# Performance work log

Hardware: AMD Instinct MI355X
Metric: run time of the kernel (lower is better)

## Reference

```python
import jax, jax.numpy as jnp
import numpy as np

ALPHA = 1.0
GAMMA = 2.0
BETA = 0.99
NUM_CLASSES = 37
N = 4_194_304


def setup_inputs() -> dict:
    key = jax.random.key(0)
    k1, k2 = jax.random.split(key)
    logits = jax.random.normal(k1, (N, NUM_CLASSES), dtype=jnp.float32)
    target = jax.random.randint(k2, (N,), 0, NUM_CLASSES, dtype=jnp.int64 if jax.config.jax_enable_x64 else jnp.int32)
    return {"logits": logits, "target": target}


def reference(logits, target):
    # Stable cross-entropy per sample: ce = -log_softmax(logits)[i, target[i]]
    logp = jax.nn.log_softmax(logits, axis=-1)                    # [N, C]
    ce = -jnp.take_along_axis(logp, target[:, None], axis=-1)[:, 0]  # [N]
    pt = jnp.exp(-ce)

    # Histogram of class counts (replaces the per-class Python loop).
    counts = jnp.zeros((NUM_CLASSES,), dtype=jnp.float32).at[target].add(1.0)  # [C]

    # Per-sample weight: 1 / beta**freq(class of sample)
    weights = (1.0 / BETA) ** counts[target]                      # [N]

    # Per-class weight: 1 / beta**(freq / total). Fresh state => total == N.
    class_weights = (1.0 / BETA) ** (counts / counts.sum())       # [C]

    focal = ALPHA * (1.0 - pt) ** GAMMA * ce * weights            # [N]
    # reduction == 'mean': (scalar / [C]).mean()
    return (focal.mean() / class_weights).mean()
```

## Files before the change

kernel.cpp:

```cpp
#include <hip/hip_runtime.h>

#define NUM_C 37
#define LOG_INV_BETA 0.010050336f
#define LOG_BETA    (-0.010050336f)
#define FLT_MAX_SAT 3.402823466e+38f

#define NBLK 2048
#define NSLOT 32
#define SLOT_PITCH 40
#define WS_CNT 64
#define WS_P   (WS_CNT + NSLOT * SLOT_PITCH)
#define WS_TOTAL (WS_P + NSLOT * SLOT_PITCH)

typedef float vf4 __attribute__((ext_vector_type(4), aligned(4)));

__device__ __forceinline__ float finite_scrub(float v, float sat) {
    unsigned u = __float_as_uint(v);
    if ((u & 0x7f800000u) == 0x7f800000u) return sat;
    return v;
}

__global__ __launch_bounds__(256) void fused_main(const float* __restrict__ logits,
                                                  const int* __restrict__ target,
                                                  float* __restrict__ ws,
                                                  int n) {
    __shared__ float hP[NUM_C];
    __shared__ unsigned hC[NUM_C];

    const int tid = threadIdx.x;
    if (tid < NUM_C) { hP[tid] = 0.0f; hC[tid] = 0u; }
    __syncthreads();

    const int lane = tid & 63;
    const int wave = (blockIdx.x << 2) | (tid >> 6);
    const int nwaves = gridDim.x << 2;
    const int total_tiles = (n + 63) >> 6;

    for (int tile = wave; tile < total_tiles; tile += nwaves) {
        long long s = ((long long)tile << 6) + lane;
        if (s < n) {
            const float* row = logits + s * NUM_C;
            int t = target[s];
            if ((unsigned)t >= NUM_C) t = 0;

            float s0 = 0.0f, s1 = 0.0f, s2 = 0.0f, s3 = 0.0f;
#pragma unroll
            for (int k = 0; k < 9; ++k) {
                vf4 v = *(const vf4*)(row + 4 * k);
                s0 += __expf(v.x);
                s1 += __expf(v.y);
                s2 += __expf(v.z);
                s3 += __expf(v.w);
            }
            float x36 = row[36];
            float sum = ((s0 + s1) + (s2 + s3)) + __expf(x36);

            float xt = row[t];
            float ce = __logf(sum) - xt;
            float pt = __expf(-ce);
            float om = 1.0f - pt;
            float term = fminf(fmaxf(om * om * ce, 0.0f), 1e30f);
            atomicAdd(&hP[t], term);
            atomicAdd(&hC[t], 1u);
        }
    }

    __syncthreads();
    if (tid < NUM_C) {
        int slot = blockIdx.x & (NSLOT - 1);
        atomicAdd(&ws[WS_CNT + slot * SLOT_PITCH + tid], (float)hC[tid]);
        atomicAdd(&ws[WS_P   + slot * SLOT_PITCH + tid], hP[tid]);
    }
}

__global__ void finalize_kernel(const float* __restrict__ ws, float* __restrict__ out, int n) {
    int c = threadIdx.x;
    float cnt = 0.0f, P = 0.0f;
    if (c < NUM_C) {
#pragma unroll
        for (int sidx = 0; sidx < NSLOT; ++sidx) {
            cnt += ws[WS_CNT + sidx * SLOT_PITCH + c];
            P   += ws[WS_P   + sidx * SLOT_PITCH + c];
        }
    }
    float e = (c < NUM_C) ? cnt * LOG_INV_BETA : 0.0f;
    float E = e;
#pragma unroll
    for (int off = 32; off > 0; off >>= 1) E = fmaxf(E, __shfl_xor(E, off, 64));
    float term = (c < NUM_C) ? P * __expf(fminf(e - E, 0.0f)) : 0.0f;
    float S = term;
#pragma unroll
    for (int off = 32; off > 0; off >>= 1) S += __shfl_xor(S, off, 64);
    float total = cnt;
#pragma unroll
    for (int off = 32; off > 0; off >>= 1) total += __shfl_xor(total, off, 64);
    total = fmaxf(total, 1.0f);
    float cw = (c < NUM_C) ? __expf((cnt / total) * LOG_BETA) : 0.0f;
    float s = cw;
#pragma unroll
    for (int off = 32; off > 0; off >>= 1) s += __shfl_xor(s, off, 64);
    if (c == 0) {
        float Sf = finite_scrub(S, 1e30f);
        float Ef = fminf(fmaxf(finite_scrub(E, 1e6f), 0.0f), 1e6f);
        float log_result = Ef + __logf(fmaxf(Sf, 1e-38f) / (float)n)
                              + __logf(fmaxf(s, 1e-38f) / (float)NUM_C);
        float v = __expf(fminf(log_result, 88.0f));
        if (log_result < -103.0f) v = 0.0f;
        v = finite_scrub(v, FLT_MAX_SAT);
        v = fminf(fmaxf(v, 0.0f), FLT_MAX_SAT);
        out[0] = v;
    }
}

extern "C" void kernel_launch(void* const* d_in, const int* in_sizes, int n_in,
                              void* d_out, int out_size, void* d_ws, size_t ws_size,
                              hipStream_t stream) {
    const float* logits = (const float*)d_in[0];
    const int* target   = (const int*)d_in[1];
    float* out          = (float*)d_out;
    float* ws           = (float*)d_ws;
    int n = in_sizes[1];

    hipMemsetAsync(d_ws, 0, WS_TOTAL * sizeof(float), stream);

    int total_tiles = (n + 63) >> 6;
    int nblocks = (total_tiles + 3) >> 2;
    if (nblocks > NBLK) nblocks = NBLK;
    if (nblocks < 1) nblocks = 1;
    fused_main<<<nblocks, 256, 0, stream>>>(logits, target, ws, n);

    finalize_kernel<<<1, 64, 0, stream>>>(ws, out, n);
}
```

Before: 787.5 us.

## Stage logit tiles through LDS with coalesced loads and register prefetch

Replaces per-thread strided row reads, where each lane reads its own 148-byte row, with block-cooperative coalesced 16-byte loads of a 256-row tile into shared memory. Each thread then computes its row's softmax from LDS. The next tile is prefetched into registers while the current one is processed, overlapping global loads with compute. This costs about 37 KB of LDS per block, two barriers per tile, a smaller grid, and likely LDS bank conflicts from the stride-37 row reads.

Measured after the change: 792.7 us. No clear change (+0.7%).

```diff
diff --git a/kernel.cpp b/kernel.cpp
--- a/kernel.cpp
+++ b/kernel.cpp
@@ -5,14 +5,16 @@
 #define LOG_BETA    (-0.010050336f)
 #define FLT_MAX_SAT 3.402823466e+38f
 
-#define NBLK 2048
+#define NBLK 1024
+#define TILE 256
+#define TILE_DW (TILE * NUM_C)
 #define NSLOT 32
 #define SLOT_PITCH 40
 #define WS_CNT 64
 #define WS_P   (WS_CNT + NSLOT * SLOT_PITCH)
 #define WS_TOTAL (WS_P + NSLOT * SLOT_PITCH)
 
-typedef float vf4 __attribute__((ext_vector_type(4), aligned(4)));
+typedef float vf4 __attribute__((ext_vector_type(4)));
 
 __device__ __forceinline__ float finite_scrub(float v, float sat) {
     unsigned u = __float_as_uint(v);
@@ -24,6 +26,7 @@
                                                   const int* __restrict__ target,
                                                   float* __restrict__ ws,
                                                   int n) {
+    __shared__ float tileb[TILE_DW];
     __shared__ float hP[NUM_C];
     __shared__ unsigned hC[NUM_C];
 
@@ -31,41 +34,106 @@
     if (tid < NUM_C) { hP[tid] = 0.0f; hC[tid] = 0u; }
     __syncthreads();
 
-    const int lane = tid & 63;
-    const int wave = (blockIdx.x << 2) | (tid >> 6);
-    const int nwaves = gridDim.x << 2;
-    const int total_tiles = (n + 63) >> 6;
-
-    for (int tile = wave; tile < total_tiles; tile += nwaves) {
-        long long s = ((long long)tile << 6) + lane;
-        if (s < n) {
-            const float* row = logits + s * NUM_C;
-            int t = target[s];
+    const int ntiles = (n + TILE - 1) >> 8;
+    float r[NUM_C + 3];
+    int t = 0;
+
+    int tile = blockIdx.x;
+    if (tile < ntiles) {
+        const float* p = logits + (long long)tile * TILE_DW;
+        bool full = (((long long)tile + 1) << 8) <= (long long)n;
+        if (full) {
+#pragma unroll
+            for (int c = 0; c < 9; ++c) {
+                vf4 v = *(const vf4*)(p + c * 1024 + tid * 4);
+                r[4 * c] = v.x; r[4 * c + 1] = v.y; r[4 * c + 2] = v.z; r[4 * c + 3] = v.w;
+            }
+            r[36] = p[9216 + tid];
+        } else {
+            int limit = (int)((long long)n - ((long long)tile << 8)) * NUM_C;
+#pragma unroll
+            for (int c = 0; c < 9; ++c) {
+#pragma unroll
+                for (int q = 0; q < 4; ++q) {
+                    int bi = c * 1024 + tid * 4 + q;
+                    r[4 * c + q] = (bi < limit) ? p[bi] : 0.0f;
+                }
+            }
+            int bi = 9216 + tid;
+            r[36] = (bi < limit) ? p[bi] : 0.0f;
+        }
+        long long sb = ((long long)tile << 8) + tid;
+        t = (sb < n) ? target[sb] : 0;
+        if ((unsigned)t >= NUM_C) t = 0;
+    }
+
+    while (tile < ntiles) {
+#pragma unroll
+        for (int c = 0; c < 9; ++c) {
+            tileb[c * 1024 + tid * 4 + 0] = r[4 * c + 0];
+            tileb[c * 1024 + tid * 4 + 1] = r[4 * c + 1];
+            tileb[c * 1024 + tid * 4 + 2] = r[4 * c + 2];
+            tileb[c * 1024 + tid * 4 + 3] = r[4 * c + 3];
+        }
+        tileb[9216 + tid] = r[36];
+        const int tc = t;
+        const int rem = (int)((((long long)n - ((long long)tile << 8)) < TILE)
+                                  ? ((long long)n - ((long long)tile << 8)) : TILE);
+        __syncthreads();
+
+        const int next = tile + gridDim.x;
+        if (next < ntiles) {
+            const float* p = logits + (long long)next * TILE_DW;
+            bool full = (((long long)next + 1) << 8) <= (long long)n;
+            if (full) {
+#pragma unroll
+                for (int c = 0; c < 9; ++c) {
+                    vf4 v = *(const vf4*)(p + c * 1024 + tid * 4);
+                    r[4 * c] = v.x; r[4 * c + 1] = v.y; r[4 * c + 2] = v.z; r[4 * c + 3] = v.w;
+                }
+                r[36] = p[9216 + tid];
+            } else {
+                int limit = (int)((long long)n - ((long long)next << 8)) * NUM_C;
+#pragma unroll
+                for (int c = 0; c < 9; ++c) {
+#pragma unroll
+                    for (int q = 0; q < 4; ++q) {
+                        int bi = c * 1024 + tid * 4 + q;
+                        r[4 * c + q] = (bi < limit) ? p[bi] : 0.0f;
+                    }
+                }
+                int bi = 9216 + tid;
+                r[36] = (bi < limit) ? p[bi] : 0.0f;
+            }
+            long long sb = ((long long)next << 8) + tid;
+            t = (sb < n) ? target[sb] : 0;
             if ((unsigned)t >= NUM_C) t = 0;
-
+        }
+
+        if (tid < rem) {
+            const float* row = &tileb[tid * NUM_C];
             float s0 = 0.0f, s1 = 0.0f, s2 = 0.0f, s3 = 0.0f;
 #pragma unroll
-            for (int k = 0; k < 9; ++k) {
-                vf4 v = *(const vf4*)(row + 4 * k);
-                s0 += __expf(v.x);
-                s1 += __expf(v.y);
-                s2 += __expf(v.z);
-                s3 += __expf(v.w);
-            }
-            float x36 = row[36];
-            float sum = ((s0 + s1) + (s2 + s3)) + __expf(x36);
-
-            float xt = row[t];
+            for (int j = 0; j < 36; j += 4) {
+                s0 += __expf(row[j]);
+                s1 += __expf(row[j + 1]);
+                s2 += __expf(row[j + 2]);
+                s3 += __expf(row[j + 3]);
+            }
+            float sum = ((s0 + s1) + (s2 + s3)) + __expf(row[36]);
+            float xt = row[tc];
             float ce = __logf(sum) - xt;
             float pt = __expf(-ce);
             float om = 1.0f - pt;
             float term = fminf(fmaxf(om * om * ce, 0.0f), 1e30f);
-            atomicAdd(&hP[t], term);
-            atomicAdd(&hC[t], 1u);
-        }
-    }
-
-    __syncthreads();
+            atomicAdd(&hP[tc], term);
+            atomicAdd(&hC[tc], 1u);
+        }
+
+        __syncthreads();
+        tile = next;
+    }
+
     if (tid < NUM_C) {
         int slot = blockIdx.x & (NSLOT - 1);
         atomicAdd(&ws[WS_CNT + slot * SLOT_PITCH + tid], (float)hC[tid]);
@@ -123,9 +191,8 @@
 
     hipMemsetAsync(d_ws, 0, WS_TOTAL * sizeof(float), stream);
 
-    int total_tiles = (n + 63) >> 6;
-    int nblocks = (total_tiles + 3) >> 2;
-    if (nblocks > NBLK) nblocks = NBLK;
+    int ntiles = (n + TILE - 1) >> 8;
+    int nblocks = ntiles < NBLK ? ntiles : NBLK;
     if (nblocks < 1) nblocks = 1;
     fused_main<<<nblocks, 256, 0, stream>>>(logits, target, ws, n);
 
```
